# Optimization experiments

Measured on AMD Instinct MI355X. Metric: run time of the kernel, lower is better.

Reference implementation:

```python
import jax, jax.numpy as jnp
import numpy as np

COST_CLASS, COST_MASK, COST_DICE = 2.0, 5.0, 5.0
NUM_POINTS = 12544

def setup_inputs() -> dict:
    key = jax.random.key(0)
    k1, k2, k3, k4, k5 = jax.random.split(key, 5)
    bs, Q, K = 4, 100, 134
    H = W = 256
    M = 80
    P = H * W
    pred_logits = jax.random.normal(k1, (bs, Q, K), dtype=jnp.float32)
    pred_masks = jax.random.normal(k2, (bs, Q, H, W), dtype=jnp.float32)
    tgt_labels = jax.random.randint(k3, (M,), 0, K - 1, dtype=jnp.int32)
    # binary target masks, stored as float (matches .float() in torch code)
    tgt_masks = (jax.random.uniform(k4, (M, H, W)) > 0.5).astype(jnp.float32)
    # random subset of points without replacement (torch.randperm[:num_points])
    point_idx = jax.random.permutation(k5, P)[:NUM_POINTS].astype(jnp.int32)
    return {"pred_logits": pred_logits, "pred_masks": pred_masks,
            "tgt_labels": tgt_labels, "tgt_masks": tgt_masks,
            "point_idx": point_idx}

def reference(pred_logits, pred_masks, tgt_labels, tgt_masks, point_idx):
    bs, Q, K = pred_logits.shape
    N = bs * Q
    M = tgt_masks.shape[0]
    Pn = point_idx.shape[0]

    # class cost: -p[n, tgt_id[m]]
    out_prob = jax.nn.softmax(pred_logits.reshape(N, K), axis=-1)
    tgt_ids = jnp.clip(tgt_labels.astype(jnp.int32), 0, K - 1)
    cost_class = -out_prob[:, tgt_ids]                      # (N, M)

    # sampled mask logits / targets
    x = pred_masks.reshape(N, -1)[:, point_idx]             # (N, Pn) logits
    y = tgt_masks.reshape(M, -1)[:, point_idx]              # (M, Pn) binary float

    # BCE-with-logits cost, separable form:
    # mean_p[softplus(x) - x*y] = mean_p softplus(x) - (x @ y^T)/Pn
    sp_mean = jnp.mean(jax.nn.softplus(x), axis=-1)         # (N,)
    xy = jnp.einsum('np,mp->nm', x, y)                      # (N, M)
    cost_mask = sp_mean[:, None] - xy / Pn

    # dice cost
    s = jax.nn.sigmoid(x)                                   # (N, Pn)
    numer = 2.0 * jnp.einsum('np,mp->nm', s, y)             # (N, M)
    denom = jnp.sum(s, axis=-1)[:, None] + jnp.sum(y, axis=-1)[None, :]
    cost_dice = 1.0 - (numer + 1.0) / (denom + 1.0)

    C = COST_CLASS * cost_class + COST_MASK * cost_mask + COST_DICE * cost_dice
    return C.reshape(bs, Q, M)
```

## Files before the change

kernel.cpp:

```cpp
#include <hip/hip_runtime.h>
#include <math.h>

#define N_ROWS 400
#define M_ROWS 80
#define K_CLS  134
#define PN     12544
#define PFULL  65536
#define WORDS  (PFULL / 32)
#define NSUB   25
#define KS     32
#define TCH    (WORDS / KS)
#define NM     (N_ROWS * M_ROWS)
#define YTCH   256

typedef __attribute__((ext_vector_type(4))) float  f32x4;
typedef __attribute__((ext_vector_type(8))) __bf16 bf16x8;

__device__ __forceinline__ float wave_reduce_sum(float v) {
#pragma unroll
    for (int off = 32; off > 0; off >>= 1) v += __shfl_down(v, off, 64);
    return v;
}

__global__ __launch_bounds__(1024) void sort_softmax_kernel(
        const int* __restrict__ point_idx,
        unsigned int* __restrict__ bitmap_g,
        const float* __restrict__ pred_logits,
        float* __restrict__ rowmax, float* __restrict__ rowsum) {
    int tid = threadIdx.x;
    if (blockIdx.x == 0) {
        __shared__ unsigned int bits[WORDS];
        bits[tid] = 0u; bits[tid + 1024] = 0u;
        __syncthreads();
        for (int i = tid; i < PN; i += 1024) {
            int p = point_idx[i];
            atomicOr(&bits[p >> 5], 1u << (p & 31));
        }
        __syncthreads();
        bitmap_g[tid]        = bits[tid];
        bitmap_g[tid + 1024] = bits[tid + 1024];
    } else {
        int wave = tid >> 6, lane = tid & 63;
        int n = (blockIdx.x - 1) * 16 + wave;
        const float* row = pred_logits + n * K_CLS;
        float mx = -1e30f;
        for (int k = lane; k < K_CLS; k += 64) mx = fmaxf(mx, row[k]);
#pragma unroll
        for (int off = 32; off > 0; off >>= 1) mx = fmaxf(mx, __shfl_down(mx, off, 64));
        mx = __shfl(mx, 0, 64);
        float se = 0.f;
        for (int k = lane; k < K_CLS; k += 64) se += expf(row[k] - mx);
        se = wave_reduce_sum(se);
        if (lane == 0) { rowmax[n] = mx; rowsum[n] = se; }
    }
}

__global__ __launch_bounds__(512) void buildY_kernel(
        const float* __restrict__ tgt_masks,
        const unsigned int* __restrict__ bitmap_g,
        bf16x8* __restrict__ Yb, float* __restrict__ ypart) {
    __shared__ float smem[128];
    int b = blockIdx.x;
    int j = b >> 8, tch = b & 255;
    int wave = threadIdx.x >> 6, lane = threadIdx.x & 63;
    int colL = lane & 15, quad = lane >> 4;
    int t = tch * 8 + wave;
    unsigned int w = bitmap_g[t];
    bf16x8 v;
    if (j < 5) {
        int m = 16 * j + colL;
        const float* yrow = tgt_masks + (size_t)m * PFULL + t * 32 + quad * 8;
        f32x4 ya = *(const f32x4*)(yrow);
        f32x4 yc = *(const f32x4*)(yrow + 4);
        float acc = 0.f;
#pragma unroll
        for (int jj = 0; jj < 4; ++jj) {
            float va = ((w >> (quad * 8 + jj)) & 1u)     ? (ya[jj] > 0.5f ? 1.f : 0.f) : 0.f;
            float vc = ((w >> (quad * 8 + jj + 4)) & 1u) ? (yc[jj] > 0.5f ? 1.f : 0.f) : 0.f;
            v[jj] = (__bf16)va; v[jj + 4] = (__bf16)vc;
            acc += va + vc;
        }
        Yb[((size_t)t * 6 + j) * 64 + lane] = v;
        acc += __shfl_down(acc, 32, 64);
        acc += __shfl_down(acc, 16, 64);
        if (quad == 0) smem[wave * 16 + colL] = acc;
        __syncthreads();
        if (threadIdx.x < 16) {
            float s = 0.f;
#pragma unroll
            for (int wv = 0; wv < 8; ++wv) s += smem[wv * 16 + threadIdx.x];
            ypart[tch * M_ROWS + 16 * j + threadIdx.x] = s;
        }
    } else {
#pragma unroll
        for (int jj = 0; jj < 8; ++jj) {
            float sv = (colL == 0 && ((w >> (quad * 8 + jj)) & 1u)) ? 1.f : 0.f;
            v[jj] = (__bf16)sv;
        }
        Yb[((size_t)t * 6 + 5) * 64 + lane] = v;
    }
}

__global__ __launch_bounds__(256) void gemm_full_kernel(
        const float* __restrict__ pred_masks,
        const bf16x8* __restrict__ Yb,
        float* __restrict__ xypart, float* __restrict__ sypart,
        float* __restrict__ rowS, float* __restrict__ rowSP) {
    __shared__ float red[4][20][64];
    __shared__ float rS[4][16], rSP[4][16];
    int tid = threadIdx.x;
    int wave = tid >> 6, lane = tid & 63;
    int colL = lane & 15, quad = lane >> 4;
    int nsub = blockIdx.x % NSUB, ch = blockIdx.x / NSUB;
    int n0 = nsub * 16;
    int t0 = ch * TCH + wave * 16;
    const float* rowp = pred_masks + (size_t)(n0 + colL) * PFULL;
    int kbase = t0 * 32 + quad * 8;

    f32x4 accX[5], accS[5];
    f32x4 zero = {0.f, 0.f, 0.f, 0.f};
#pragma unroll
    for (int j = 0; j < 5; ++j) { accX[j] = zero; accS[j] = zero; }
    f32x4 acc5S = zero, acc5P = zero;

    f32x4 pa0 = *(const f32x4*)(rowp + kbase);
    f32x4 pb0 = *(const f32x4*)(rowp + kbase + 4);
    f32x4 pa1 = *(const f32x4*)(rowp + kbase + 32);
    f32x4 pb1 = *(const f32x4*)(rowp + kbase + 36);

#pragma unroll
    for (int i = 0; i < 16; ++i) {
        const bf16x8* q = Yb + ((size_t)(t0 + i) * 6) * 64 + lane;
        bf16x8 B0 = q[0], B1 = q[64], B2 = q[128], B3 = q[192], B4 = q[256], B5 = q[320];
        f32x4 xa = pa0, xb = pb0;
        pa0 = pa1; pb0 = pb1;
        if (i < 14) {
            pa1 = *(const f32x4*)(rowp + kbase + (i + 2) * 32);
            pb1 = *(const f32x4*)(rowp + kbase + (i + 2) * 32 + 4);
        }
        float xsv[8];
        *(f32x4*)(xsv) = xa; *(f32x4*)(xsv + 4) = xb;
        bf16x8 aX, aS, aSP;
#pragma unroll
        for (int jj = 0; jj < 8; ++jj) {
            float x  = xsv[jj];
            float ax = fabsf(x);
            float e  = __expf(-ax);
            float inv = __builtin_amdgcn_rcpf(1.f + e);
            float sig = (x >= 0.f) ? inv : e * inv;
            float sp  = fmaxf(x, 0.f) + __logf(1.f + e);
            aX[jj] = (__bf16)x; aS[jj] = (__bf16)sig; aSP[jj] = (__bf16)sp;
        }
        accX[0] = __builtin_amdgcn_mfma_f32_16x16x32_bf16(aX, B0, accX[0], 0, 0, 0);
        accS[0] = __builtin_amdgcn_mfma_f32_16x16x32_bf16(aS, B0, accS[0], 0, 0, 0);
        accX[1] = __builtin_amdgcn_mfma_f32_16x16x32_bf16(aX, B1, accX[1], 0, 0, 0);
        accS[1] = __builtin_amdgcn_mfma_f32_16x16x32_bf16(aS, B1, accS[1], 0, 0, 0);
        accX[2] = __builtin_amdgcn_mfma_f32_16x16x32_bf16(aX, B2, accX[2], 0, 0, 0);
        accS[2] = __builtin_amdgcn_mfma_f32_16x16x32_bf16(aS, B2, accS[2], 0, 0, 0);
        accX[3] = __builtin_amdgcn_mfma_f32_16x16x32_bf16(aX, B3, accX[3], 0, 0, 0);
        accS[3] = __builtin_amdgcn_mfma_f32_16x16x32_bf16(aS, B3, accS[3], 0, 0, 0);
        accX[4] = __builtin_amdgcn_mfma_f32_16x16x32_bf16(aX, B4, accX[4], 0, 0, 0);
        accS[4] = __builtin_amdgcn_mfma_f32_16x16x32_bf16(aS, B4, accS[4], 0, 0, 0);
        acc5S   = __builtin_amdgcn_mfma_f32_16x16x32_bf16(aS,  B5, acc5S, 0, 0, 0);
        acc5P   = __builtin_amdgcn_mfma_f32_16x16x32_bf16(aSP, B5, acc5P, 0, 0, 0);
    }

#pragma unroll
    for (int j = 0; j < 5; ++j)
#pragma unroll
        for (int r = 0; r < 4; ++r) red[wave][j * 4 + r][lane] = accX[j][r];
    if (colL == 0) {
#pragma unroll
        for (int r = 0; r < 4; ++r) {
            rS[wave][quad * 4 + r]  = acc5S[r];
            rSP[wave][quad * 4 + r] = acc5P[r];
        }
    }
    __syncthreads();
#pragma unroll
    for (int v0 = 0; v0 < 5; ++v0) {
        int v = wave * 5 + v0;
        float s = red[0][v][lane] + red[1][v][lane] + red[2][v][lane] + red[3][v][lane];
        int j = v >> 2, r = v & 3;
        int n = n0 + quad * 4 + r, m = 16 * j + colL;
        xypart[(size_t)ch * NM + n * M_ROWS + m] = s;
    }
    if (tid < 16) {
        rowS[ch * N_ROWS + n0 + tid] = rS[0][tid] + rS[1][tid] + rS[2][tid] + rS[3][tid];
    } else if (tid < 32) {
        int l = tid - 16;
        rowSP[ch * N_ROWS + n0 + l] = rSP[0][l] + rSP[1][l] + rSP[2][l] + rSP[3][l];
    }
    __syncthreads();
#pragma unroll
    for (int j = 0; j < 5; ++j)
#pragma unroll
        for (int r = 0; r < 4; ++r) red[wave][j * 4 + r][lane] = accS[j][r];
    __syncthreads();
#pragma unroll
    for (int v0 = 0; v0 < 5; ++v0) {
        int v = wave * 5 + v0;
        float s = red[0][v][lane] + red[1][v][lane] + red[2][v][lane] + red[3][v][lane];
        int j = v >> 2, r = v & 3;
        int n = n0 + quad * 4 + r, m = 16 * j + colL;
        sypart[(size_t)ch * NM + n * M_ROWS + m] = s;
    }
}

__global__ void combine_kernel(const float* __restrict__ logits,
                               const int* __restrict__ tgt_labels,
                               const float* __restrict__ rowmax,
                               const float* __restrict__ rowsum,
                               const float* __restrict__ rowS,
                               const float* __restrict__ rowSP,
                               const float* __restrict__ ypart,
                               const float* __restrict__ xypart,
                               const float* __restrict__ sypart,
                               float* __restrict__ out) {
    int idx = blockIdx.x * blockDim.x + threadIdx.x;
    if (idx >= NM) return;
    int n = idx / M_ROWS, m = idx % M_ROWS;
    float xy = 0.f, sy = 0.f, ssumv = 0.f, spsumv = 0.f, ysum = 0.f;
#pragma unroll 8
    for (int g = 0; g < KS; ++g) {
        xy += xypart[(size_t)g * NM + idx];
        sy += sypart[(size_t)g * NM + idx];
        ssumv  += rowS[g * N_ROWS + n];
        spsumv += rowSP[g * N_ROWS + n];
    }
#pragma unroll 16
    for (int g = 0; g < YTCH; ++g) ysum += ypart[g * M_ROWS + m];
    int tid = tgt_labels[m];
    tid = min(max(tid, 0), K_CLS - 1);
    float p = expf(logits[n * K_CLS + tid] - rowmax[n]) / rowsum[n];
    float cost_class = -p;
    float cost_mask = (spsumv - xy) * (1.0f / PN);
    float cost_dice = 1.f - (2.f * sy + 1.f) / (ssumv + ysum + 1.f);
    out[idx] = 2.f * cost_class + 5.f * cost_mask + 5.f * cost_dice;
}

extern "C" void kernel_launch(void* const* d_in, const int* in_sizes, int n_in,
                              void* d_out, int out_size, void* d_ws, size_t ws_size,
                              hipStream_t stream) {
    const float* pred_logits = (const float*)d_in[0];
    const float* pred_masks  = (const float*)d_in[1];
    const int*   tgt_labels  = (const int*)d_in[2];
    const float* tgt_masks   = (const float*)d_in[3];
    const int*   point_idx   = (const int*)d_in[4];
    float* out = (float*)d_out;

    char* ws = (char*)d_ws;
    size_t off = 0;
    auto carve = [&](size_t nbytes) {
        char* p = ws + off;
        off += (nbytes + 255) & ~(size_t)255;
        return p;
    };
    unsigned int* bitmap = (unsigned int*)carve(WORDS * 4);
    bf16x8* Yb    = (bf16x8*)carve((size_t)WORDS * 6 * 64 * 16);
    float* rowmax = (float*)carve(N_ROWS * 4);
    float* rowsum = (float*)carve(N_ROWS * 4);
    float* ypart  = (float*)carve((size_t)YTCH * M_ROWS * 4);
    float* rowS   = (float*)carve((size_t)KS * N_ROWS * 4);
    float* rowSP  = (float*)carve((size_t)KS * N_ROWS * 4);
    float* xypart = (float*)carve((size_t)KS * NM * 4);
    float* sypart = (float*)carve((size_t)KS * NM * 4);
    (void)ws_size; (void)in_sizes; (void)n_in; (void)out_size;

    sort_softmax_kernel<<<26, 1024, 0, stream>>>(point_idx, bitmap,
                                                 pred_logits, rowmax, rowsum);
    buildY_kernel<<<6 * YTCH, 512, 0, stream>>>(tgt_masks, bitmap, Yb, ypart);
    gemm_full_kernel<<<NSUB * KS, 256, 0, stream>>>(
        pred_masks, Yb, xypart, sypart, rowS, rowSP);
    combine_kernel<<<(NM + 255) / 256, 256, 0, stream>>>(
        pred_logits, tgt_labels, rowmax, rowsum, rowS, rowSP, ypart,
        xypart, sypart, out);
}
```

Measured before the change: 222.2 us.

## Double KS split, deepen prefetch pipeline, and register-buffer Y tiles in GEMM

Doubles the number of K-chunks, so each wave runs 8 iterations instead of 16 and the grid has twice as many blocks. The prediction-mask prefetch goes from two stages to three, and the next iteration's B operand tiles are loaded into registers one step ahead. A min-blocks-per-SM hint of 4 is added to launch bounds. This aims to hide global load latency and raise parallelism, at the cost of more partial sums to reduce downstream and higher register pressure.

```diff
diff --git a/kernel.cpp b/kernel.cpp
--- a/kernel.cpp
+++ b/kernel.cpp
@@ -8,8 +8,9 @@
 #define PFULL  65536
 #define WORDS  (PFULL / 32)
 #define NSUB   25
-#define KS     32
+#define KS     64
 #define TCH    (WORDS / KS)
+#define ITERS  (TCH / 4)
 #define NM     (N_ROWS * M_ROWS)
 #define YTCH   256
 
@@ -101,7 +102,7 @@
     }
 }
 
-__global__ __launch_bounds__(256) void gemm_full_kernel(
+__global__ __launch_bounds__(256, 4) void gemm_full_kernel(
         const float* __restrict__ pred_masks,
         const bf16x8* __restrict__ Yb,
         float* __restrict__ xypart, float* __restrict__ sypart,
@@ -113,7 +114,7 @@
     int colL = lane & 15, quad = lane >> 4;
     int nsub = blockIdx.x % NSUB, ch = blockIdx.x / NSUB;
     int n0 = nsub * 16;
-    int t0 = ch * TCH + wave * 16;
+    int t0 = ch * TCH + wave * ITERS;
     const float* rowp = pred_masks + (size_t)(n0 + colL) * PFULL;
     int kbase = t0 * 32 + quad * 8;
 
@@ -123,20 +124,32 @@
     for (int j = 0; j < 5; ++j) { accX[j] = zero; accS[j] = zero; }
     f32x4 acc5S = zero, acc5P = zero;
 
-    f32x4 pa0 = *(const f32x4*)(rowp + kbase);
-    f32x4 pb0 = *(const f32x4*)(rowp + kbase + 4);
-    f32x4 pa1 = *(const f32x4*)(rowp + kbase + 32);
-    f32x4 pb1 = *(const f32x4*)(rowp + kbase + 36);
-
-#pragma unroll
-    for (int i = 0; i < 16; ++i) {
-        const bf16x8* q = Yb + ((size_t)(t0 + i) * 6) * 64 + lane;
-        bf16x8 B0 = q[0], B1 = q[64], B2 = q[128], B3 = q[192], B4 = q[256], B5 = q[320];
-        f32x4 xa = pa0, xb = pb0;
-        pa0 = pa1; pb0 = pb1;
-        if (i < 14) {
-            pa1 = *(const f32x4*)(rowp + kbase + (i + 2) * 32);
-            pb1 = *(const f32x4*)(rowp + kbase + (i + 2) * 32 + 4);
+    f32x4 PA[3], PB[3];
+#pragma unroll
+    for (int d = 0; d < 3; ++d) {
+        PA[d] = *(const f32x4*)(rowp + kbase + d * 32);
+        PB[d] = *(const f32x4*)(rowp + kbase + d * 32 + 4);
+    }
+    bf16x8 Bc[6], Bn[6];
+    {
+        const bf16x8* q = Yb + ((size_t)t0 * 6) * 64 + lane;
+#pragma unroll
+        for (int j = 0; j < 6; ++j) Bc[j] = q[j * 64];
+    }
+
+#pragma unroll
+    for (int i = 0; i < ITERS; ++i) {
+        if (i + 1 < ITERS) {
+            const bf16x8* q = Yb + ((size_t)(t0 + i + 1) * 6) * 64 + lane;
+#pragma unroll
+            for (int j = 0; j < 6; ++j) Bn[j] = q[j * 64];
+        }
+        f32x4 xa = PA[0], xb = PB[0];
+        PA[0] = PA[1]; PB[0] = PB[1];
+        PA[1] = PA[2]; PB[1] = PB[2];
+        if (i + 3 < ITERS) {
+            PA[2] = *(const f32x4*)(rowp + kbase + (i + 3) * 32);
+            PB[2] = *(const f32x4*)(rowp + kbase + (i + 3) * 32 + 4);
         }
         float xsv[8];
         *(f32x4*)(xsv) = xa; *(f32x4*)(xsv + 4) = xb;
@@ -146,23 +159,26 @@
             float x  = xsv[jj];
             float ax = fabsf(x);
             float e  = __expf(-ax);
-            float inv = __builtin_amdgcn_rcpf(1.f + e);
+            float den = 1.f + e;
+            float inv = __builtin_amdgcn_rcpf(den);
             float sig = (x >= 0.f) ? inv : e * inv;
-            float sp  = fmaxf(x, 0.f) + __logf(1.f + e);
+            float sp  = fmaxf(x, 0.f) + __logf(den);
             aX[jj] = (__bf16)x; aS[jj] = (__bf16)sig; aSP[jj] = (__bf16)sp;
         }
-        accX[0] = __builtin_amdgcn_mfma_f32_16x16x32_bf16(aX, B0, accX[0], 0, 0, 0);
-        accS[0] = __builtin_amdgcn_mfma_f32_16x16x32_bf16(aS, B0, accS[0], 0, 0, 0);
-        accX[1] = __builtin_amdgcn_mfma_f32_16x16x32_bf16(aX, B1, accX[1], 0, 0, 0);
-        accS[1] = __builtin_amdgcn_mfma_f32_16x16x32_bf16(aS, B1, accS[1], 0, 0, 0);
-        accX[2] = __builtin_amdgcn_mfma_f32_16x16x32_bf16(aX, B2, accX[2], 0, 0, 0);
-        accS[2] = __builtin_amdgcn_mfma_f32_16x16x32_bf16(aS, B2, accS[2], 0, 0, 0);
-        accX[3] = __builtin_amdgcn_mfma_f32_16x16x32_bf16(aX, B3, accX[3], 0, 0, 0);
-        accS[3] = __builtin_amdgcn_mfma_f32_16x16x32_bf16(aS, B3, accS[3], 0, 0, 0);
-        accX[4] = __builtin_amdgcn_mfma_f32_16x16x32_bf16(aX, B4, accX[4], 0, 0, 0);
-        accS[4] = __builtin_amdgcn_mfma_f32_16x16x32_bf16(aS, B4, accS[4], 0, 0, 0);
-        acc5S   = __builtin_amdgcn_mfma_f32_16x16x32_bf16(aS,  B5, acc5S, 0, 0, 0);
-        acc5P   = __builtin_amdgcn_mfma_f32_16x16x32_bf16(aSP, B5, acc5P, 0, 0, 0);
+        accX[0] = __builtin_amdgcn_mfma_f32_16x16x32_bf16(aX, Bc[0], accX[0], 0, 0, 0);
+        accS[0] = __builtin_amdgcn_mfma_f32_16x16x32_bf16(aS, Bc[0], accS[0], 0, 0, 0);
+        accX[1] = __builtin_amdgcn_mfma_f32_16x16x32_bf16(aX, Bc[1], accX[1], 0, 0, 0);
+        accS[1] = __builtin_amdgcn_mfma_f32_16x16x32_bf16(aS, Bc[1], accS[1], 0, 0, 0);
+        accX[2] = __builtin_amdgcn_mfma_f32_16x16x32_bf16(aX, Bc[2], accX[2], 0, 0, 0);
+        accS[2] = __builtin_amdgcn_mfma_f32_16x16x32_bf16(aS, Bc[2], accS[2], 0, 0, 0);
+        accX[3] = __builtin_amdgcn_mfma_f32_16x16x32_bf16(aX, Bc[3], accX[3], 0, 0, 0);
+        accS[3] = __builtin_amdgcn_mfma_f32_16x16x32_bf16(aS, Bc[3], accS[3], 0, 0, 0);
+        accX[4] = __builtin_amdgcn_mfma_f32_16x16x32_bf16(aX, Bc[4], accX[4], 0, 0, 0);
+        accS[4] = __builtin_amdgcn_mfma_f32_16x16x32_bf16(aS, Bc[4], accS[4], 0, 0, 0);
+        acc5S   = __builtin_amdgcn_mfma_f32_16x16x32_bf16(aS,  Bc[5], acc5S, 0, 0, 0);
+        acc5P   = __builtin_amdgcn_mfma_f32_16x16x32_bf16(aSP, Bc[5], acc5P, 0, 0, 0);
+#pragma unroll
+        for (int j = 0; j < 6; ++j) Bc[j] = Bn[j];
     }
 
 #pragma unroll
```

Result: no change. 219.5 us (-1.2%).
